# Kernel optimization log

Measured on AMD Instinct MI355X. Metric: run time of the kernel, lower is better.

The kernel has to match this reference:

```python
import jax, jax.numpy as jnp
import numpy as np

N_NODES = 100000
N_EDGES = 1600000
IN_DIM, HID_DIM, N_CLASSES = 128, 64, 40


def spmm(edge_row, edge_col, edge_val, dense):
    # sparse [N,N] @ dense [N,D] via gather + segment-sum over edges
    msgs = edge_val[:, None] * dense[edge_col]            # [E, D]
    return jax.ops.segment_sum(msgs, edge_row, num_segments=N_NODES)


def setup_inputs() -> dict:
    key = jax.random.key(0)
    ks = jax.random.split(key, 8)
    x = jax.random.normal(ks[0], (N_NODES, IN_DIM), dtype=jnp.float32)
    edge_row = jax.random.randint(ks[1], (N_EDGES,), 0, N_NODES, dtype=jnp.int32)
    edge_col = jax.random.randint(ks[2], (N_EDGES,), 0, N_NODES, dtype=jnp.int32)
    edge_val = jax.random.uniform(ks[3], (N_EDGES,), dtype=jnp.float32)
    s1 = 1.0 / np.sqrt(IN_DIM)
    s2 = 1.0 / np.sqrt(HID_DIM)
    W1 = jax.random.normal(ks[4], (IN_DIM, HID_DIM), dtype=jnp.float32) * s1
    b1 = jnp.zeros((HID_DIM,), dtype=jnp.float32)
    W2 = jax.random.normal(ks[5], (HID_DIM, HID_DIM), dtype=jnp.float32) * s2
    b2 = jnp.zeros((HID_DIM,), dtype=jnp.float32)
    Wc = jax.random.normal(ks[6], (HID_DIM, N_CLASSES), dtype=jnp.float32) * s2
    bc = jnp.zeros((N_CLASSES,), dtype=jnp.float32)
    return {"x": x, "edge_row": edge_row, "edge_col": edge_col, "edge_val": edge_val,
            "W1": W1, "b1": b1, "W2": W2, "b2": b2, "Wc": Wc, "bc": bc}


def reference(x, edge_row, edge_col, edge_val, W1, b1, W2, b2, Wc, bc):
    # GCN layer 1: support = xW+b, aggregate, relu  (dropout off in eval)
    h = jax.nn.relu(spmm(edge_row, edge_col, edge_val, x @ W1 + b1))
    # GCN layer 2
    h = spmm(edge_row, edge_col, edge_val, h @ W2 + b2)
    # node classifier + log-softmax
    logits = h @ Wc + bc
    return jax.nn.log_softmax(logits, axis=-1)
```

## Files before the change

kernel.cpp:

```cpp
#include <hip/hip_runtime.h>

#define N_NODES   100000
#define N_EDGES   1600000
#define IN_DIM    128
#define HID_DIM   64
#define N_CLASSES 40
#define U_DIM     40

#define NBUCK 782
#define BCAP  2816
#define EPB   6400
#define PBLK  1024
#define GRID_A 250

typedef __attribute__((ext_vector_type(8))) short bf16x8;
typedef __attribute__((ext_vector_type(4))) float f32x4;

__device__ inline short f2bf(float f) {
    unsigned u = __float_as_uint(f);
    unsigned r = (u + 0x7FFFu + ((u >> 16) & 1u)) >> 16;
    return (short)r;
}
__device__ inline float bflo(unsigned w) { return __uint_as_float(w << 16); }
__device__ inline float bfhi(unsigned w) { return __uint_as_float(w & 0xFFFF0000u); }
__device__ inline float upval(unsigned w) { return __uint_as_float((w >> 17) << 16); }

__global__ __launch_bounds__(PBLK) void prep_parta(const int* __restrict__ erow,
                                                   const int* __restrict__ ecol,
                                                   const float* __restrict__ eval,
                                                   int* __restrict__ bcnt,
                                                   int2* __restrict__ tmp,
                                                   const float* __restrict__ W1,
                                                   const float* __restrict__ W2,
                                                   const float* __restrict__ Wc,
                                                   const float* __restrict__ b2,
                                                   short* __restrict__ W1t,
                                                   short* __restrict__ Mt,
                                                   float* __restrict__ bv) {
    __shared__ int2 pay[EPB];
    __shared__ int hist[NBUCK], lbase[NBUCK], cur[NBUCK], dofs[NBUCK], scan[NBUCK];
    int tid = threadIdx.x;
    if (blockIdx.x >= GRID_A) {
        int pb = blockIdx.x - GRID_A;
        {
            int i = pb * PBLK + tid;
            if (i < IN_DIM * HID_DIM) {
                int n = i >> 7, k = i & 127;
                W1t[i] = f2bf(W1[k * HID_DIM + n]);
            }
        }
        if (pb == 0) {
            for (int idx = tid; idx < HID_DIM * HID_DIM; idx += PBLK) {
                int n = idx >> 6, i = idx & 63;
                float acc = 0.f;
                if (n < N_CLASSES)
                    for (int j = 0; j < HID_DIM; ++j)
                        acc = fmaf(W2[i * HID_DIM + j], Wc[j * N_CLASSES + n], acc);
                Mt[n * HID_DIM + i] = f2bf(acc);
            }
        }
        if (pb == 1 && tid < N_CLASSES) {
            float acc = 0.f;
            for (int j = 0; j < HID_DIM; ++j)
                acc = fmaf(b2[j], Wc[j * N_CLASSES + tid], acc);
            bv[tid] = acc;
        }
        return;
    }
    int e0 = blockIdx.x * EPB;
    for (int i = tid; i < NBUCK; i += PBLK) { hist[i] = 0; cur[i] = 0; }
    __syncthreads();
    for (int i = tid; i < EPB; i += PBLK)
        atomicAdd(&hist[erow[e0 + i] >> 7], 1);
    __syncthreads();
    for (int i = tid; i < NBUCK; i += PBLK) {
        int n = hist[i];
        dofs[i] = i * BCAP + (n ? atomicAdd(&bcnt[i], n) : 0);
        scan[i] = n;
    }
    __syncthreads();
    for (int off = 1; off < NBUCK; off <<= 1) {
        int t = 0;
        if (tid < NBUCK && tid >= off) t = scan[tid - off];
        __syncthreads();
        if (tid < NBUCK) scan[tid] += t;
        __syncthreads();
    }
    if (tid < NBUCK) {
        lbase[tid] = scan[tid] - hist[tid];
        dofs[tid] -= lbase[tid];
    }
    __syncthreads();
    for (int i = tid; i < EPB; i += PBLK) {
        int e = e0 + i;
        int r = erow[e];
        int b = r >> 7;
        int p = lbase[b] + atomicAdd(&cur[b], 1);
        unsigned u = __float_as_uint(eval[e]);
        unsigned vb = ((u + 0x7FFFu + ((u >> 16) & 1u)) >> 16) & 0x7FFFu;
        pay[p] = make_int2(((r & 127) << 17) | ecol[e], (int)((vb << 10) | (unsigned)b));
    }
    __syncthreads();
    for (int p = tid; p < EPB; p += PBLK) {
        int2 v = pay[p];
        int b = (unsigned)v.y & 1023u;
        int dest = dofs[b] + p;
        if (dest < (b + 1) * BCAP)
            tmp[dest] = v;
    }
}

__global__ __launch_bounds__(256) void part_b_gemm1(const int* __restrict__ bcnt,
                                                    const int2* __restrict__ tmp,
                                                    unsigned* __restrict__ tmp2,
                                                    int2* __restrict__ rowmeta,
                                                    const float* __restrict__ x,
                                                    const short* __restrict__ W1t,
                                                    const float* __restrict__ b1,
                                                    unsigned short* __restrict__ outH) {
    __shared__ int2 ein[BCAP];
    __shared__ unsigned eout[BCAP];
    __shared__ int hist[128], pad[128], basep[128], cur[128], scan[128];
    if (blockIdx.x < NBUCK) {
        int b = blockIdx.x;
        int nb = bcnt[b]; if (nb > BCAP) nb = BCAP;
        for (int i = threadIdx.x; i < nb; i += 256) ein[i] = tmp[(size_t)b * BCAP + i];
        if (threadIdx.x < 128) { hist[threadIdx.x] = 0; cur[threadIdx.x] = 0; }
        __syncthreads();
        for (int i = threadIdx.x; i < nb; i += 256)
            atomicAdd(&hist[(ein[i].x >> 17) & 127], 1);
        __syncthreads();
        if (threadIdx.x < 128) {
            pad[threadIdx.x] = (hist[threadIdx.x] + 3) & ~3;
            scan[threadIdx.x] = pad[threadIdx.x];
        }
        __syncthreads();
        for (int off = 1; off < 128; off <<= 1) {
            int t = 0;
            if (threadIdx.x < 128 && threadIdx.x >= off) t = scan[threadIdx.x - off];
            __syncthreads();
            if (threadIdx.x < 128) scan[threadIdx.x] += t;
            __syncthreads();
        }
        if (threadIdx.x < 128) basep[threadIdx.x] = scan[threadIdx.x] - pad[threadIdx.x];
        __syncthreads();
        int ntot = scan[127]; if (ntot > BCAP) ntot = BCAP;
        for (int i = threadIdx.x; i < nb; i += 256) {
            int lr = (ein[i].x >> 17) & 127;
            int p = basep[lr] + atomicAdd(&cur[lr], 1);
            if (p < BCAP) {
                unsigned vb = ((unsigned)ein[i].y >> 10) & 0x7FFFu;
                eout[p] = (vb << 17) | (unsigned)(ein[i].x & 0x1FFFF);
            }
        }
        __syncthreads();
        if (threadIdx.x < 128) {
            int pe = basep[threadIdx.x] + pad[threadIdx.x];
            for (int p = basep[threadIdx.x] + hist[threadIdx.x]; p < pe && p < BCAP; ++p)
                eout[p] = 0u;
        }
        __syncthreads();
        for (int i = threadIdx.x; i < ntot; i += 256) tmp2[(size_t)b * BCAP + i] = eout[i];
        if (threadIdx.x < 128) {
            int r = b * 128 + threadIdx.x;
            if (r < N_NODES)
                rowmeta[r] = make_int2(b * BCAP + basep[threadIdx.x], pad[threadIdx.x]);
        }
    } else {
        int gb = blockIdx.x - NBUCK;
        int wave = threadIdx.x >> 6;
        int lane = threadIdx.x & 63;
        int node0 = gb * 64 + wave * 16;
        if (node0 >= N_NODES) return;
        int m = lane & 15;
        int q = lane >> 4;
        const float* xrow = x + (size_t)(node0 + m) * IN_DIM;
        f32x4 acc0 = {0,0,0,0}, acc1 = {0,0,0,0}, acc2 = {0,0,0,0}, acc3 = {0,0,0,0};
#pragma unroll
        for (int kb = 0; kb < 4; ++kb) {
            int k0 = kb * 32 + q * 8;
            float4 a0 = *(const float4*)(xrow + k0);
            float4 a1 = *(const float4*)(xrow + k0 + 4);
            bf16x8 af;
            af[0]=f2bf(a0.x); af[1]=f2bf(a0.y); af[2]=f2bf(a0.z); af[3]=f2bf(a0.w);
            af[4]=f2bf(a1.x); af[5]=f2bf(a1.y); af[6]=f2bf(a1.z); af[7]=f2bf(a1.w);
            bf16x8 bf0 = *(const bf16x8*)(W1t + ( 0 + m) * IN_DIM + k0);
            bf16x8 bf1 = *(const bf16x8*)(W1t + (16 + m) * IN_DIM + k0);
            bf16x8 bf2 = *(const bf16x8*)(W1t + (32 + m) * IN_DIM + k0);
            bf16x8 bf3 = *(const bf16x8*)(W1t + (48 + m) * IN_DIM + k0);
            acc0 = __builtin_amdgcn_mfma_f32_16x16x32_bf16(af, bf0, acc0, 0, 0, 0);
            acc1 = __builtin_amdgcn_mfma_f32_16x16x32_bf16(af, bf1, acc1, 0, 0, 0);
            acc2 = __builtin_amdgcn_mfma_f32_16x16x32_bf16(af, bf2, acc2, 0, 0, 0);
            acc3 = __builtin_amdgcn_mfma_f32_16x16x32_bf16(af, bf3, acc3, 0, 0, 0);
        }
        f32x4 accs[4] = {acc0, acc1, acc2, acc3};
#pragma unroll
        for (int t = 0; t < 4; ++t) {
            float bias = b1[t * 16 + m];
#pragma unroll
            for (int r = 0; r < 4; ++r) {
                int node = node0 + q * 4 + r;
                outH[(size_t)node * HID_DIM + t * 16 + m] = (unsigned short)f2bf(accs[t][r] + bias);
            }
        }
    }
}

#define FMA8(v,g) \
    a0=fmaf(v,bflo(g.x),a0); a1=fmaf(v,bfhi(g.x),a1); a2=fmaf(v,bflo(g.y),a2); a3=fmaf(v,bfhi(g.y),a3); \
    a4=fmaf(v,bflo(g.z),a4); a5=fmaf(v,bfhi(g.z),a5); a6=fmaf(v,bflo(g.w),a6); a7=fmaf(v,bfhi(g.w),a7);

__global__ __launch_bounds__(256) void spmm1_mm(const int2* __restrict__ rowmeta,
                                                const unsigned* __restrict__ ecv,
                                                const unsigned short* __restrict__ dense,
                                                const short* __restrict__ Mt,
                                                unsigned short* __restrict__ outU) {
    __shared__ unsigned lm[4][8][68];
    __shared__ unsigned short tr[32][64];
    int wave = threadIdx.x >> 6;
    int lane = threadIdx.x & 63;
    int s = lane >> 3, dq = lane & 7;
    int row = wave * 8 + s;
    int r = blockIdx.x * 32 + row;
    int2 meta = rowmeta[r];
    int beg = meta.x, deg = meta.y;
    int degc = deg < 64 ? deg : 64;
    for (int e = dq * 2; e < degc; e += 16)
        *(uint2*)&lm[wave][s][e] = *(const uint2*)(ecv + beg + e);
    __syncthreads();
    const unsigned* mp = lm[wave][s];
    float a0=0,a1=0,a2=0,a3=0,a4=0,a5=0,a6=0,a7=0;
#define LDG(wv) (*(const uint4*)(dense + ((size_t)((wv) & 0x1FFFF) << 6) + (dq << 3)))
    if (deg > 0) {
        int e = 0;
        if (degc & 4) {
            uint4 w = *(const uint4*)mp;
            uint4 g0 = LDG(w.x), g1 = LDG(w.y), g2 = LDG(w.z), g3 = LDG(w.w);
            float v0 = upval(w.x), v1 = upval(w.y), v2 = upval(w.z), v3 = upval(w.w);
            FMA8(v0,g0); FMA8(v1,g1); FMA8(v2,g2); FMA8(v3,g3);
            e = 4;
        }
        for (; e < degc; e += 8) {
            uint4 wa = *(const uint4*)(mp + e);
            uint4 wb = *(const uint4*)(mp + e + 4);
            uint4 g0 = LDG(wa.x), g1 = LDG(wa.y), g2 = LDG(wa.z), g3 = LDG(wa.w);
            uint4 g4 = LDG(wb.x), g5 = LDG(wb.y), g6 = LDG(wb.z), g7 = LDG(wb.w);
            float v0 = upval(wa.x), v1 = upval(wa.y), v2 = upval(wa.z), v3 = upval(wa.w);
            float v4 = upval(wb.x), v5 = upval(wb.y), v6 = upval(wb.z), v7 = upval(wb.w);
            FMA8(v0,g0); FMA8(v1,g1); FMA8(v2,g2); FMA8(v3,g3);
            FMA8(v4,g4); FMA8(v5,g5); FMA8(v6,g6); FMA8(v7,g7);
        }
        for (int e2 = 64; e2 < deg; ++e2) {
            unsigned we = ecv[beg + e2];
            uint4 g = LDG(we);
            float v = upval(we);
            FMA8(v,g);
        }
    }
#undef LDG
    uint4 o;
    o.x = (unsigned short)f2bf(fmaxf(a0,0.f)) | ((unsigned)(unsigned short)f2bf(fmaxf(a1,0.f)) << 16);
    o.y = (unsigned short)f2bf(fmaxf(a2,0.f)) | ((unsigned)(unsigned short)f2bf(fmaxf(a3,0.f)) << 16);
    o.z = (unsigned short)f2bf(fmaxf(a4,0.f)) | ((unsigned)(unsigned short)f2bf(fmaxf(a5,0.f)) << 16);
    o.w = (unsigned short)f2bf(fmaxf(a6,0.f)) | ((unsigned)(unsigned short)f2bf(fmaxf(a7,0.f)) << 16);
    *(uint4*)(&tr[row][(dq ^ s) << 3]) = o;
    __syncthreads();
    int m = lane & 15;
    int q = lane >> 4;
    int nt = wave >> 1;
    int tb = (wave & 1) << 1;
    int arow = nt * 16 + m;
    f32x4 c0 = {0,0,0,0}, c1 = {0,0,0,0};
#pragma unroll
    for (int kb = 0; kb < 2; ++kb) {
        int ch = kb * 4 + q;
        bf16x8 af = *(const bf16x8*)(&tr[arow][(ch ^ (arow & 7)) << 3]);
        int k0 = kb * 32 + q * 8;
        bf16x8 bf0 = *(const bf16x8*)(Mt + ((tb + 0) * 16 + m) * HID_DIM + k0);
        bf16x8 bf1 = *(const bf16x8*)(Mt + ((tb + 1) * 16 + m) * HID_DIM + k0);
        c0 = __builtin_amdgcn_mfma_f32_16x16x32_bf16(af, bf0, c0, 0, 0, 0);
        c1 = __builtin_amdgcn_mfma_f32_16x16x32_bf16(af, bf1, c1, 0, 0, 0);
    }
#pragma unroll
    for (int rr = 0; rr < 4; ++rr) {
        int node = blockIdx.x * 32 + nt * 16 + q * 4 + rr;
        int col0 = tb * 16 + m;
        int col1 = col0 + 16;
        if (col0 < U_DIM)
            outU[(size_t)node * U_DIM + col0] = (unsigned short)f2bf(c0[rr]);
        if (col1 < U_DIM)
            outU[(size_t)node * U_DIM + col1] = (unsigned short)f2bf(c1[rr]);
    }
}

__global__ __launch_bounds__(256) void spmm_cls(const int2* __restrict__ rowmeta,
                                                const unsigned* __restrict__ ecv,
                                                const unsigned short* __restrict__ dense,
                                                const float* __restrict__ bv,
                                                const float* __restrict__ bc,
                                                float* __restrict__ outF) {
    __shared__ unsigned lm[4][8][68];
    int wave = threadIdx.x >> 6;
    int lane = threadIdx.x & 63;
    int s = lane >> 3, dq = lane & 7;
    int dof = (dq < 5 ? dq : 0) << 3;
    int r = (blockIdx.x * 4 + wave) * 8 + s;
    float4 bv0 = {0,0,0,0}, bv1 = {0,0,0,0}, bc0 = {0,0,0,0}, bc1 = {0,0,0,0};
    if (dq < 5) {
        bv0 = *(const float4*)(bv + dq * 8);  bv1 = *(const float4*)(bv + dq * 8 + 4);
        bc0 = *(const float4*)(bc + dq * 8);  bc1 = *(const float4*)(bc + dq * 8 + 4);
    }
    int2 meta = rowmeta[r];
    int beg = meta.x, deg = meta.y;
    int degc = deg < 64 ? deg : 64;
    for (int e = dq * 2; e < degc; e += 16)
        *(uint2*)&lm[wave][s][e] = *(const uint2*)(ecv + beg + e);
    __syncthreads();
    const unsigned* mp = lm[wave][s];
    float a0=0,a1=0,a2=0,a3=0,a4=0,a5=0,a6=0,a7=0, asum=0;
#define LDU(wv) (*(const uint4*)(dense + (size_t)((wv) & 0x1FFFF) * U_DIM + dof))
    if (deg > 0) {
        int e = 0;
        if (degc & 4) {
            uint4 w = *(const uint4*)mp;
            uint4 g0 = LDU(w.x), g1 = LDU(w.y), g2 = LDU(w.z), g3 = LDU(w.w);
            float v0 = upval(w.x), v1 = upval(w.y), v2 = upval(w.z), v3 = upval(w.w);
            asum += v0 + v1 + v2 + v3;
            FMA8(v0,g0); FMA8(v1,g1); FMA8(v2,g2); FMA8(v3,g3);
            e = 4;
        }
        for (; e < degc; e += 8) {
            uint4 wa = *(const uint4*)(mp + e);
            uint4 wb = *(const uint4*)(mp + e + 4);
            uint4 g0 = LDU(wa.x), g1 = LDU(wa.y), g2 = LDU(wa.z), g3 = LDU(wa.w);
            uint4 g4 = LDU(wb.x), g5 = LDU(wb.y), g6 = LDU(wb.z), g7 = LDU(wb.w);
            float v0 = upval(wa.x), v1 = upval(wa.y), v2 = upval(wa.z), v3 = upval(wa.w);
            float v4 = upval(wb.x), v5 = upval(wb.y), v6 = upval(wb.z), v7 = upval(wb.w);
            asum += v0 + v1 + v2 + v3 + v4 + v5 + v6 + v7;
            FMA8(v0,g0); FMA8(v1,g1); FMA8(v2,g2); FMA8(v3,g3);
            FMA8(v4,g4); FMA8(v5,g5); FMA8(v6,g6); FMA8(v7,g7);
        }
        for (int e2 = 64; e2 < deg; ++e2) {
            unsigned we = ecv[beg + e2];
            uint4 g = LDU(we);
            float v = upval(we);
            asum += v;
            FMA8(v,g);
        }
    }
#undef LDU
    float l0 = fmaf(asum, bv0.x, a0) + bc0.x;
    float l1 = fmaf(asum, bv0.y, a1) + bc0.y;
    float l2 = fmaf(asum, bv0.z, a2) + bc0.z;
    float l3 = fmaf(asum, bv0.w, a3) + bc0.w;
    float l4 = fmaf(asum, bv1.x, a4) + bc1.x;
    float l5 = fmaf(asum, bv1.y, a5) + bc1.y;
    float l6 = fmaf(asum, bv1.z, a6) + bc1.z;
    float l7 = fmaf(asum, bv1.w, a7) + bc1.w;
    float mx = -1e30f;
    if (dq < 5)
        mx = fmaxf(fmaxf(fmaxf(l0, l1), fmaxf(l2, l3)),
                   fmaxf(fmaxf(l4, l5), fmaxf(l6, l7)));
#pragma unroll
    for (int off = 1; off < 8; off <<= 1) mx = fmaxf(mx, __shfl_xor(mx, off));
    float ss = 0.f;
    if (dq < 5)
        ss = __expf(l0 - mx) + __expf(l1 - mx) + __expf(l2 - mx) + __expf(l3 - mx)
           + __expf(l4 - mx) + __expf(l5 - mx) + __expf(l6 - mx) + __expf(l7 - mx);
#pragma unroll
    for (int off = 1; off < 8; off <<= 1) ss += __shfl_xor(ss, off);
    float lse = mx + __logf(ss);
    if (dq < 5) {
        float4 o0 = {l0 - lse, l1 - lse, l2 - lse, l3 - lse};
        float4 o1 = {l4 - lse, l5 - lse, l6 - lse, l7 - lse};
        float* dst = outF + (size_t)r * N_CLASSES + dq * 8;
        *(float4*)(dst) = o0;
        *(float4*)(dst + 4) = o1;
    }
}

extern "C" void kernel_launch(void* const* d_in, const int* in_sizes, int n_in,
                              void* d_out, int out_size, void* d_ws, size_t ws_size,
                              hipStream_t stream) {
    const float* x    = (const float*)d_in[0];
    const int*   erow = (const int*)  d_in[1];
    const int*   ecol = (const int*)  d_in[2];
    const float* eval = (const float*)d_in[3];
    const float* W1   = (const float*)d_in[4];
    const float* b1   = (const float*)d_in[5];
    const float* W2   = (const float*)d_in[6];
    const float* b2   = (const float*)d_in[7];
    const float* Wc   = (const float*)d_in[8];
    const float* bc   = (const float*)d_in[9];
    float* out = (float*)d_out;

    char* ws = (char*)d_ws;
    size_t off = 0;
    auto alloc = [&](size_t bytes) { char* p = ws + off; off += (bytes + 255) & ~(size_t)255; return p; };
    unsigned short* bufA = (unsigned short*)alloc((size_t)N_NODES * HID_DIM * sizeof(short));
    unsigned short* bufB = (unsigned short*)alloc((size_t)N_NODES * U_DIM * sizeof(short));
    int2*     tmp     = (int2*)    alloc((size_t)NBUCK * BCAP * sizeof(int2));
    unsigned* tmp2    = (unsigned*)alloc((size_t)NBUCK * BCAP * sizeof(unsigned));
    int2*     rowmeta = (int2*)    alloc((size_t)N_NODES * sizeof(int2));
    int*      bcnt    = (int*)     alloc(NBUCK * sizeof(int));
    short*    W1t     = (short*)   alloc((size_t)IN_DIM * HID_DIM * sizeof(short));
    short*    Mt      = (short*)   alloc((size_t)HID_DIM * HID_DIM * sizeof(short));
    float*    bv      = (float*)   alloc(64 * sizeof(float));

    const int tile_grid = (N_NODES + 63) / 64;
    const int spmm_grid = N_NODES / 32;

    hipMemsetAsync(bcnt, 0, NBUCK * sizeof(int), stream);
    prep_parta<<<GRID_A + 8, PBLK, 0, stream>>>(erow, ecol, eval, bcnt, tmp,
                                                W1, W2, Wc, b2, W1t, Mt, bv);
    part_b_gemm1<<<NBUCK + tile_grid, 256, 0, stream>>>(bcnt, tmp, tmp2, rowmeta,
                                                        x, W1t, b1, bufA);
    spmm1_mm<<<spmm_grid, 256, 0, stream>>>(rowmeta, tmp2, bufA, Mt, bufB);
    spmm_cls<<<spmm_grid, 256, 0, stream>>>(rowmeta, tmp2, bufB, bv, bc, out);
}
```

Before: 218.4 us.

## Sort rows by padded degree within each bucket to balance SpMM wave work

After: 226.3 us. +3.6%, slower.

```diff
diff --git a/kernel.cpp b/kernel.cpp
--- a/kernel.cpp
+++ b/kernel.cpp
@@ -162,9 +162,18 @@
         __syncthreads();
         for (int i = threadIdx.x; i < ntot; i += 256) tmp2[(size_t)b * BCAP + i] = eout[i];
         if (threadIdx.x < 128) {
-            int r = b * 128 + threadIdx.x;
-            if (r < N_NODES)
-                rowmeta[r] = make_int2(b * BCAP + basep[threadIdx.x], pad[threadIdx.x]);
+            int nvalid = N_NODES - b * 128; if (nvalid > 128) nvalid = 128;
+            int lr = threadIdx.x;
+            if (lr < nvalid) {
+                int mypad = pad[lr];
+                int rank = 0;
+                for (int j = 0; j < nvalid; ++j) {
+                    int pj = pad[j];
+                    rank += (pj < mypad) || (pj == mypad && j < lr);
+                }
+                rowmeta[b * 128 + rank] =
+                    make_int2(b * BCAP + basep[lr], (mypad << 17) | (b * 128 + lr));
+            }
         }
     } else {
         int gb = blockIdx.x - NBUCK;
@@ -217,16 +226,19 @@
                                                 unsigned short* __restrict__ outU) {
     __shared__ unsigned lm[4][8][68];
     __shared__ unsigned short tr[32][64];
+    __shared__ int rid[32];
     int wave = threadIdx.x >> 6;
     int lane = threadIdx.x & 63;
     int s = lane >> 3, dq = lane & 7;
     int row = wave * 8 + s;
-    int r = blockIdx.x * 32 + row;
-    int2 meta = rowmeta[r];
-    int beg = meta.x, deg = meta.y;
+    int slot = blockIdx.x * 32 + row;
+    int2 meta = rowmeta[slot];
+    int beg = meta.x;
+    int deg = (int)(((unsigned)meta.y) >> 17);
+    if (dq == 0) rid[row] = meta.y & 0x1FFFF;
     int degc = deg < 64 ? deg : 64;
-    for (int e = dq * 2; e < degc; e += 16)
-        *(uint2*)&lm[wave][s][e] = *(const uint2*)(ecv + beg + e);
+    for (int e = dq; e < degc; e += 8)
+        lm[wave][s][e] = ecv[beg + e];
     __syncthreads();
     const unsigned* mp = lm[wave][s];
     float a0=0,a1=0,a2=0,a3=0,a4=0,a5=0,a6=0,a7=0;
@@ -283,7 +295,7 @@
     }
 #pragma unroll
     for (int rr = 0; rr < 4; ++rr) {
-        int node = blockIdx.x * 32 + nt * 16 + q * 4 + rr;
+        int node = rid[nt * 16 + q * 4 + rr];
         int col0 = tb * 16 + m;
         int col1 = col0 + 16;
         if (col0 < U_DIM)
@@ -304,17 +316,19 @@
     int lane = threadIdx.x & 63;
     int s = lane >> 3, dq = lane & 7;
     int dof = (dq < 5 ? dq : 0) << 3;
-    int r = (blockIdx.x * 4 + wave) * 8 + s;
+    int slot = (blockIdx.x * 4 + wave) * 8 + s;
     float4 bv0 = {0,0,0,0}, bv1 = {0,0,0,0}, bc0 = {0,0,0,0}, bc1 = {0,0,0,0};
     if (dq < 5) {
         bv0 = *(const float4*)(bv + dq * 8);  bv1 = *(const float4*)(bv + dq * 8 + 4);
         bc0 = *(const float4*)(bc + dq * 8);  bc1 = *(const float4*)(bc + dq * 8 + 4);
     }
-    int2 meta = rowmeta[r];
-    int beg = meta.x, deg = meta.y;
+    int2 meta = rowmeta[slot];
+    int beg = meta.x;
+    int deg = (int)(((unsigned)meta.y) >> 17);
+    int r   = meta.y & 0x1FFFF;
     int degc = deg < 64 ? deg : 64;
-    for (int e = dq * 2; e < degc; e += 16)
-        *(uint2*)&lm[wave][s][e] = *(const uint2*)(ecv + beg + e);
+    for (int e = dq; e < degc; e += 8)
+        lm[wave][s][e] = ecv[beg + e];
     __syncthreads();
     const unsigned* mp = lm[wave][s];
     float a0=0,a1=0,a2=0,a3=0,a4=0,a5=0,a6=0,a7=0, asum=0;
```
